# Optimization experiments

Measured on AMD Instinct MI355X. Metric: run time of the kernel, lower is better.

The kernel has to match this reference:

```python
import jax, jax.numpy as jnp
import numpy as np

B, T, I, H, V = 32, 64, 512, 512, 32000


def setup_inputs() -> dict:
    key = jax.random.key(0)
    ks = jax.random.split(key, 8)
    s_in = 1.0 / np.sqrt(H)  # torch LSTMCell/Linear uniform init scale
    return {
        "isequence": jax.random.normal(ks[0], (B, T, I), dtype=jnp.float32),
        "hidden_t": jax.random.normal(ks[1], (B, H), dtype=jnp.float32),
        "W_ih": jax.random.uniform(ks[2], (4 * H, I), jnp.float32, -s_in, s_in),
        "W_hh": jax.random.uniform(ks[3], (4 * H, H), jnp.float32, -s_in, s_in),
        "b_ih": jax.random.uniform(ks[4], (4 * H,), jnp.float32, -s_in, s_in),
        "b_hh": jax.random.uniform(ks[5], (4 * H,), jnp.float32, -s_in, s_in),
        "W_out": jax.random.uniform(ks[6], (V, H), jnp.float32, -s_in, s_in),
        "b_out": jax.random.uniform(ks[7], (V,), jnp.float32, -s_in, s_in),
    }


def reference(isequence, hidden_t, W_ih, W_hh, b_ih, b_hh, W_out, b_out):
    # isequence: [B, T, I] -> time-major [T, B, I] (matches permute(1,0,2))
    xs = jnp.transpose(isequence, (1, 0, 2))
    # Precompute input-to-gate projections for all timesteps: [T, B, 4H]
    x_gates = jnp.einsum("tbi,gi->tbg", xs, W_ih) + b_ih + b_hh
    c0 = jnp.zeros_like(hidden_t)  # init_hidden zeros cell state

    def step(carry, xg):
        h, c = carry
        gates = xg + h @ W_hh.T  # [B, 4H], torch gate order: i, f, g, o
        i_g, f_g, g_g, o_g = jnp.split(gates, 4, axis=-1)
        i_g = jax.nn.sigmoid(i_g)
        f_g = jax.nn.sigmoid(f_g)
        g_g = jnp.tanh(g_g)
        o_g = jax.nn.sigmoid(o_g)
        c_new = f_g * c + i_g * g_g
        h_new = o_g * jnp.tanh(c_new)
        logits = h_new @ W_out.T + b_out  # [B, V]
        return (h_new, c_new), logits

    _, osequence = jax.lax.scan(step, (hidden_t, c0), x_gates)  # [T, B, V]
    return jnp.transpose(osequence, (1, 0, 2))  # [B, T, V]
```

## Files before the change

### kernel.cpp

```cpp
#include <hip/hip_runtime.h>
#include <hip/hip_bf16.h>

typedef unsigned short u16;
typedef unsigned int u32;
typedef __attribute__((ext_vector_type(4))) float f32x4;
typedef __attribute__((ext_vector_type(8))) short short8;
typedef __attribute__((ext_vector_type(4))) unsigned short u16x4;
typedef __attribute__((ext_vector_type(4))) unsigned int u32x4;

#define LSTM_NBLK 16

static __device__ __forceinline__ u16 f2bf(float f) {
  union { float f; unsigned u; } v; v.f = f;
  unsigned r = v.u + 0x7FFFu + ((v.u >> 16) & 1u);
  return (u16)(r >> 16);
}

static __device__ __forceinline__ void gload_lds16(const void* g, void* l) {
  __builtin_amdgcn_global_load_lds(
      (const __attribute__((address_space(1))) unsigned int*)g,
      (__attribute__((address_space(3))) unsigned int*)l, 16, 0, 0);
}

static __device__ __forceinline__ short8 ld_b128_sc(const void* p) {
  short8 r;
  asm volatile("global_load_dwordx4 %0, %1, off sc0 sc1"
               : "=v"(r) : "v"(p) : "memory");
  return r;
}
static __device__ __forceinline__ unsigned ld_u32_sc_wait(const unsigned* p) {
  unsigned r;
  asm volatile("global_load_dword %0, %1, off sc0 sc1\n\ts_waitcnt vmcnt(0)"
               : "=v"(r) : "v"(p) : "memory");
  return r;
}
static __device__ __forceinline__ void st_u32_sc(void* p, unsigned v) {
  asm volatile("global_store_dword %0, %1, off sc0 sc1"
               :: "v"(p), "v"(v) : "memory");
}
static __device__ __forceinline__ void waitcnt0() {
  asm volatile("s_waitcnt vmcnt(0)" ::: "memory");
  __builtin_amdgcn_sched_barrier(0);
}

__global__ void prep_kernel(const float* __restrict__ iseq, const float* __restrict__ h0,
                            const float* __restrict__ wih, const float* __restrict__ whh,
                            const float* __restrict__ wout,
                            u16* __restrict__ wout_bf, u16* __restrict__ wih_bf,
                            u16* __restrict__ whh_bf, u16* __restrict__ ax,
                            u32* __restrict__ h2u, unsigned* __restrict__ flags) {
  const int S0 = 4096000;
  const int S1 = S0 + 262144;
  const int S2 = S1 + 262144;
  const int S3 = S2 + 262144;
  const int S4 = S3 + 8192;
  const int S5 = S4 + 4096;
  int u = blockIdx.x * blockDim.x + threadIdx.x;
  int stride = gridDim.x * blockDim.x;
  for (; u < S5; u += stride) {
    if (u < S0) {
      int e = u * 4; f32x4 v = *(const f32x4*)(wout + e);
      u16x4 o; o[0]=f2bf(v[0]); o[1]=f2bf(v[1]); o[2]=f2bf(v[2]); o[3]=f2bf(v[3]);
      *(u16x4*)(wout_bf + e) = o;
    } else if (u < S1) {
      int e = (u - S0) * 4; f32x4 v = *(const f32x4*)(wih + e);
      u16x4 o; o[0]=f2bf(v[0]); o[1]=f2bf(v[1]); o[2]=f2bf(v[2]); o[3]=f2bf(v[3]);
      *(u16x4*)(wih_bf + e) = o;
    } else if (u < S2) {
      int e = (u - S1) * 4; f32x4 v = *(const f32x4*)(whh + e);
      u16x4 o; o[0]=f2bf(v[0]); o[1]=f2bf(v[1]); o[2]=f2bf(v[2]); o[3]=f2bf(v[3]);
      *(u16x4*)(whh_bf + e) = o;
    } else if (u < S3) {
      int e = (u - S2) * 4; int m = e >> 9; int k = e & 511;
      int b = m & 31; int t = m >> 5;
      f32x4 v = *(const f32x4*)(iseq + ((b * 64 + t) << 9) + k);
      u16x4 o; o[0]=f2bf(v[0]); o[1]=f2bf(v[1]); o[2]=f2bf(v[2]); o[3]=f2bf(v[3]);
      *(u16x4*)(ax + e) = o;
    } else if (u < S4) {
      int v = u - S3;
      int e = v * 2;
      float lo = h0[e], hi = h0[e + 1];
      h2u[v] = (((u32)f2bf(hi)) << 16) | (u32)f2bf(lo);
    } else {
      flags[u - S4] = 0u;
    }
  }
}

__global__ __launch_bounds__(256, 2) void gemm_bt(
    const u16* __restrict__ A, const u16* __restrict__ Bw,
    float* __restrict__ C, const float* __restrict__ bias1,
    const float* __restrict__ bias2, int N, int remap) {
  __shared__ u16 As[2][8192];
  __shared__ u16 Bs[2][8192];
  const int tid = threadIdx.x;
  const int w = tid >> 6, l = tid & 63;
  const int wr = w >> 1, wc = w & 1;
  const int tm = blockIdx.y * 128, tn = blockIdx.x * 128;

  f32x4 acc[4][4];
#pragma unroll
  for (int i = 0; i < 4; ++i)
#pragma unroll
    for (int j = 0; j < 4; ++j) acc[i][j] = (f32x4){0.f, 0.f, 0.f, 0.f};

  auto stage = [&](int buf, int kt) {
#pragma unroll
    for (int i = 0; i < 4; ++i) {
      int r = (w * 4 + i) * 8 + (l >> 3);
      int c16 = (l & 7) ^ (r & 7);
      int rowm = tm + r;
      const u16* srca;
      if (remap) {
        srca = A + ((rowm & 63) + 1) * 16384 + (rowm >> 6) * 512 + kt * 64 + c16 * 8;
      } else {
        srca = A + rowm * 512 + kt * 64 + c16 * 8;
      }
      gload_lds16(srca, &As[buf][(w * 4 + i) * 512]);
      const u16* srcb = Bw + (tn + r) * 512 + kt * 64 + c16 * 8;
      gload_lds16(srcb, &Bs[buf][(w * 4 + i) * 512]);
    }
  };

  stage(0, 0);
  int buf = 0;
  for (int kt = 0; kt < 8; ++kt) {
    __syncthreads();
    if (kt < 7) stage(buf ^ 1, kt + 1);
#pragma unroll
    for (int kk = 0; kk < 2; ++kk) {
      short8 af[4], bfr[4];
#pragma unroll
      for (int mi = 0; mi < 4; ++mi) {
        int row = wr * 64 + mi * 16 + (l & 15);
        int s = (kk * 4 + (l >> 4)) ^ (row & 7);
        af[mi] = *(const short8*)&As[buf][row * 64 + s * 8];
      }
#pragma unroll
      for (int ni = 0; ni < 4; ++ni) {
        int row = wc * 64 + ni * 16 + (l & 15);
        int s = (kk * 4 + (l >> 4)) ^ (row & 7);
        bfr[ni] = *(const short8*)&Bs[buf][row * 64 + s * 8];
      }
#pragma unroll
      for (int mi = 0; mi < 4; ++mi)
#pragma unroll
        for (int ni = 0; ni < 4; ++ni)
          acc[mi][ni] = __builtin_amdgcn_mfma_f32_16x16x32_bf16(
              af[mi], bfr[ni], acc[mi][ni], 0, 0, 0);
    }
    buf ^= 1;
  }

#pragma unroll
  for (int ni = 0; ni < 4; ++ni) {
    int gcol = tn + wc * 64 + ni * 16 + (l & 15);
    float bv = 0.f;
    if (bias1) bv += bias1[gcol];
    if (bias2) bv += bias2[gcol];
#pragma unroll
    for (int mi = 0; mi < 4; ++mi) {
      int grow0 = tm + wr * 64 + mi * 16 + ((l >> 4) << 2);
      f32x4 a = acc[mi][ni];
#pragma unroll
      for (int q = 0; q < 4; ++q) {
        C[(long long)(grow0 + q) * N + gcol] = a[q] + bv;
      }
    }
  }
}

__global__ __launch_bounds__(512, 1) void lstm_persist(
    const u16* __restrict__ whh, const float* __restrict__ xg,
    u16* __restrict__ h2, unsigned* __restrict__ flags) {
  __shared__ u16 hbuf[32 * 512];
  __shared__ u16 hloc[1024];
  const int tid = threadIdx.x;
  const int w = tid >> 6, l = tid & 63;
  const int blk = blockIdx.x;
  const int j0 = (blk * 8 + w) * 4;
  const int c = l & 15;
  const int wrow = (c >> 2) * 512 + j0 + (c & 3);
  const int ko = (l >> 4) * 8;
  u32* h2u = (u32*)h2;

  short8 bfr[16];
  const u16* wp = whh + wrow * 512 + ko;
#pragma unroll
  for (int kt = 0; kt < 16; ++kt) bfr[kt] = *(const short8*)(wp + kt * 32);

  const int rq = (l >> 4) * 4;
  const int jj = l & 3;
  const int b0 = l & 15, b1 = 16 + (l & 15);
  const int s0 = b0 & 7;

  const int cb = tid & 31;
  const int ckg = tid >> 5;
  const int csw = cb & 7;

  const int ob = tid >> 4;
  const int oj = tid & 15;

  float creg[2][4];
#pragma unroll
  for (int mt = 0; mt < 2; ++mt)
#pragma unroll
    for (int q = 0; q < 4; ++q) creg[mt][q] = 0.f;

  float xcur[2][4], xnext[2][4];
#pragma unroll
  for (int mt = 0; mt < 2; ++mt)
#pragma unroll
    for (int q = 0; q < 4; ++q)
      xcur[mt][q] = xg[(mt * 16 + rq + q) * 2048 + wrow];

  for (int it = 0; it < 64; ++it) {
    if (it > 0 && w == 0) {
      const unsigned want = (unsigned)it;
      for (;;) {
        unsigned f = ld_u32_sc_wait(flags + blk * 256 + (l & 15) * 16);
        if (__all((int)(f >= want))) break;
      }
    }
    __syncthreads();

    {
      const u16* src = h2 + it * 16384 + cb * 512 + ckg * 32;
      short8 d0 = ld_b128_sc(src);
      short8 d1 = ld_b128_sc(src + 8);
      short8 d2 = ld_b128_sc(src + 16);
      short8 d3 = ld_b128_sc(src + 24);
      waitcnt0();
      *(short8*)&hbuf[cb * 512 + (((ckg * 4 + 0) ^ csw) * 8)] = d0;
      *(short8*)&hbuf[cb * 512 + (((ckg * 4 + 1) ^ csw) * 8)] = d1;
      *(short8*)&hbuf[cb * 512 + (((ckg * 4 + 2) ^ csw) * 8)] = d2;
      *(short8*)&hbuf[cb * 512 + (((ckg * 4 + 3) ^ csw) * 8)] = d3;
    }
    __syncthreads();

    f32x4 acc0 = (f32x4){0.f, 0.f, 0.f, 0.f};
    f32x4 acc1 = (f32x4){0.f, 0.f, 0.f, 0.f};
#pragma unroll
    for (int kt = 0; kt < 16; ++kt) {
      int x = ((kt * 4 + (l >> 4)) ^ s0) * 8;
      short8 a0 = *(const short8*)&hbuf[b0 * 512 + x];
      short8 a1 = *(const short8*)&hbuf[b1 * 512 + x];
      acc0 = __builtin_amdgcn_mfma_f32_16x16x32_bf16(a0, bfr[kt], acc0, 0, 0, 0);
      acc1 = __builtin_amdgcn_mfma_f32_16x16x32_bf16(a1, bfr[kt], acc1, 0, 0, 0);
    }
    if (it < 63) {
#pragma unroll
      for (int mt = 0; mt < 2; ++mt)
#pragma unroll
        for (int q = 0; q < 4; ++q)
          xnext[mt][q] = xg[((it + 1) * 32 + mt * 16 + rq + q) * 2048 + wrow];
    }

#pragma unroll
    for (int mt = 0; mt < 2; ++mt) {
#pragma unroll
      for (int q = 0; q < 4; ++q) {
        float av = (mt == 0) ? acc0[q] : acc1[q];
        float gp = av + xcur[mt][q];
        int bl = (l & 48) | jj;
        float xi = __shfl(gp, bl);
        float xf = __shfl(gp, bl | 4);
        float xgg = __shfl(gp, bl | 8);
        float xo = __shfl(gp, bl | 12);
        float is = 1.f / (1.f + __expf(-xi));
        float fs = 1.f / (1.f + __expf(-xf));
        float e2 = __expf(2.f * xgg);
        float gt = 1.f - 2.f / (e2 + 1.f);
        float os = 1.f / (1.f + __expf(-xo));
        float cn = fs * creg[mt][q] + is * gt;
        creg[mt][q] = cn;
        float e2c = __expf(2.f * cn);
        float hn = os * (1.f - 2.f / (e2c + 1.f));
        if ((l & 12) == 0) {
          int b = mt * 16 + rq + q;
          hloc[b * 32 + w * 4 + jj] = f2bf(hn);
        }
      }
    }
    __syncthreads();

    {
      u32 v = *(const u32*)&hloc[ob * 32 + oj * 2];
      st_u32_sc(h2u + (it + 1) * 8192 + ob * 256 + blk * 16 + oj, v);
      waitcnt0();
    }
    __syncthreads();

    if (it < 63) {
      if (w == 0 && l < 16)
        st_u32_sc(flags + l * 256 + blk * 16, (unsigned)(it + 1));
#pragma unroll
      for (int mt = 0; mt < 2; ++mt)
#pragma unroll
        for (int q = 0; q < 4; ++q)
          xcur[mt][q] = xnext[mt][q];
    }
  }
}

extern "C" void kernel_launch(void* const* d_in, const int* in_sizes, int n_in,
                              void* d_out, int out_size, void* d_ws, size_t ws_size,
                              hipStream_t stream) {
  (void)in_sizes; (void)n_in; (void)out_size; (void)ws_size;
  const float* iseq = (const float*)d_in[0];
  const float* h0   = (const float*)d_in[1];
  const float* wih  = (const float*)d_in[2];
  const float* whh  = (const float*)d_in[3];
  const float* bih  = (const float*)d_in[4];
  const float* bhh  = (const float*)d_in[5];
  const float* wout = (const float*)d_in[6];
  const float* bout = (const float*)d_in[7];

  char* ws = (char*)d_ws;
  u16* wout_bf = (u16*)(ws + 0);
  u16* wih_bf  = (u16*)(ws + 32768000);
  u16* whh_bf  = (u16*)(ws + 34865152);
  u16* ax      = (u16*)(ws + 36962304);
  u16* h2      = (u16*)(ws + 39059456);
  unsigned* flags = (unsigned*)(ws + 41189376);
  float* xg    = (float*)(ws + 41254912);
  float* out   = (float*)d_out;

  prep_kernel<<<4096, 256, 0, stream>>>(iseq, h0, wih, whh, wout,
                                        wout_bf, wih_bf, whh_bf, ax,
                                        (u32*)h2, flags);
  gemm_bt<<<dim3(16, 16), 256, 0, stream>>>(ax, wih_bf, xg, bih, bhh, 2048, 0);
  lstm_persist<<<LSTM_NBLK, 512, 0, stream>>>(whh_bf, xg, h2, flags);
  gemm_bt<<<dim3(250, 16), 256, 0, stream>>>(h2, wout_bf, out, bout, nullptr, 32000, 1);
}
```

Before: 575.5 us.

## Fuse output projection into persistent LSTM kernel, overlapping it with recurrence

New measurement: 779.0 us. 1.35x slower.

```diff
diff --git a/kernel.cpp b/kernel.cpp
--- a/kernel.cpp
+++ b/kernel.cpp
@@ -9,6 +9,7 @@
 typedef __attribute__((ext_vector_type(4))) unsigned int u32x4;
 
 #define LSTM_NBLK 16
+#define PROJ_NBLK 250
 
 static __device__ __forceinline__ u16 f2bf(float f) {
   union { float f; unsigned u; } v; v.f = f;
@@ -90,7 +91,7 @@
 __global__ __launch_bounds__(256, 2) void gemm_bt(
     const u16* __restrict__ A, const u16* __restrict__ Bw,
     float* __restrict__ C, const float* __restrict__ bias1,
-    const float* __restrict__ bias2, int N, int remap) {
+    const float* __restrict__ bias2, int N) {
   __shared__ u16 As[2][8192];
   __shared__ u16 Bs[2][8192];
   const int tid = threadIdx.x;
@@ -109,13 +110,7 @@
     for (int i = 0; i < 4; ++i) {
       int r = (w * 4 + i) * 8 + (l >> 3);
       int c16 = (l & 7) ^ (r & 7);
-      int rowm = tm + r;
-      const u16* srca;
-      if (remap) {
-        srca = A + ((rowm & 63) + 1) * 16384 + (rowm >> 6) * 512 + kt * 64 + c16 * 8;
-      } else {
-        srca = A + rowm * 512 + kt * 64 + c16 * 8;
-      }
+      const u16* srca = A + (tm + r) * 512 + kt * 64 + c16 * 8;
       gload_lds16(srca, &As[buf][(w * 4 + i) * 512]);
       const u16* srcb = Bw + (tn + r) * 512 + kt * 64 + c16 * 8;
       gload_lds16(srcb, &Bs[buf][(w * 4 + i) * 512]);
@@ -170,62 +165,169 @@
   }
 }
 
-__global__ __launch_bounds__(512, 1) void lstm_persist(
+__global__ __launch_bounds__(512, 1) void fused_persist(
     const u16* __restrict__ whh, const float* __restrict__ xg,
-    u16* __restrict__ h2, unsigned* __restrict__ flags) {
+    u16* __restrict__ h2, unsigned* __restrict__ flags,
+    const u16* __restrict__ woutb, const float* __restrict__ bout,
+    float* __restrict__ out) {
   __shared__ u16 hbuf[32 * 512];
   __shared__ u16 hloc[1024];
   const int tid = threadIdx.x;
   const int w = tid >> 6, l = tid & 63;
-  const int blk = blockIdx.x;
-  const int j0 = (blk * 8 + w) * 4;
-  const int c = l & 15;
-  const int wrow = (c >> 2) * 512 + j0 + (c & 3);
-  const int ko = (l >> 4) * 8;
   u32* h2u = (u32*)h2;
 
-  short8 bfr[16];
-  const u16* wp = whh + wrow * 512 + ko;
-#pragma unroll
-  for (int kt = 0; kt < 16; ++kt) bfr[kt] = *(const short8*)(wp + kt * 32);
-
-  const int rq = (l >> 4) * 4;
-  const int jj = l & 3;
-  const int b0 = l & 15, b1 = 16 + (l & 15);
-  const int s0 = b0 & 7;
+  if (blockIdx.x < LSTM_NBLK) {
+    const int blk = blockIdx.x;
+    const int j0 = (blk * 8 + w) * 4;
+    const int c = l & 15;
+    const int wrow = (c >> 2) * 512 + j0 + (c & 3);
+    const int ko = (l >> 4) * 8;
+
+    short8 bfr[16];
+    const u16* wp = whh + wrow * 512 + ko;
+#pragma unroll
+    for (int kt = 0; kt < 16; ++kt) bfr[kt] = *(const short8*)(wp + kt * 32);
+
+    const int rq = (l >> 4) * 4;
+    const int jj = l & 3;
+    const int b0 = l & 15, b1 = 16 + (l & 15);
+    const int s0 = b0 & 7;
+
+    const int cb = tid & 31;
+    const int ckg = tid >> 5;
+    const int csw = cb & 7;
+    const int ob = tid >> 4;
+    const int oj = tid & 15;
+
+    float creg[2][4];
+#pragma unroll
+    for (int mt = 0; mt < 2; ++mt)
+#pragma unroll
+      for (int q = 0; q < 4; ++q) creg[mt][q] = 0.f;
+
+    float xcur[2][4], xnext[2][4];
+#pragma unroll
+    for (int mt = 0; mt < 2; ++mt)
+#pragma unroll
+      for (int q = 0; q < 4; ++q)
+        xcur[mt][q] = xg[(mt * 16 + rq + q) * 2048 + wrow];
+
+    for (int it = 0; it < 64; ++it) {
+      if (it > 0 && w == 0) {
+        const unsigned want = (unsigned)it;
+        for (;;) {
+          unsigned f = ld_u32_sc_wait(flags + blk * 256 + (l & 15) * 16);
+          if (__all((int)(f >= want))) break;
+        }
+      }
+      __syncthreads();
+
+      {
+        const u16* src = h2 + it * 16384 + cb * 512 + ckg * 32;
+        short8 d0 = ld_b128_sc(src);
+        short8 d1 = ld_b128_sc(src + 8);
+        short8 d2 = ld_b128_sc(src + 16);
+        short8 d3 = ld_b128_sc(src + 24);
+        waitcnt0();
+        *(short8*)&hbuf[cb * 512 + (((ckg * 4 + 0) ^ csw) * 8)] = d0;
+        *(short8*)&hbuf[cb * 512 + (((ckg * 4 + 1) ^ csw) * 8)] = d1;
+        *(short8*)&hbuf[cb * 512 + (((ckg * 4 + 2) ^ csw) * 8)] = d2;
+        *(short8*)&hbuf[cb * 512 + (((ckg * 4 + 3) ^ csw) * 8)] = d3;
+      }
+      __syncthreads();
+
+      f32x4 acc0 = (f32x4){0.f, 0.f, 0.f, 0.f};
+      f32x4 acc1 = (f32x4){0.f, 0.f, 0.f, 0.f};
+#pragma unroll
+      for (int kt = 0; kt < 16; ++kt) {
+        int x = ((kt * 4 + (l >> 4)) ^ s0) * 8;
+        short8 a0 = *(const short8*)&hbuf[b0 * 512 + x];
+        short8 a1 = *(const short8*)&hbuf[b1 * 512 + x];
+        acc0 = __builtin_amdgcn_mfma_f32_16x16x32_bf16(a0, bfr[kt], acc0, 0, 0, 0);
+        acc1 = __builtin_amdgcn_mfma_f32_16x16x32_bf16(a1, bfr[kt], acc1, 0, 0, 0);
+      }
+      if (it < 63) {
+#pragma unroll
+        for (int mt = 0; mt < 2; ++mt)
+#pragma unroll
+          for (int q = 0; q < 4; ++q)
+            xnext[mt][q] = xg[((it + 1) * 32 + mt * 16 + rq + q) * 2048 + wrow];
+      }
+
+#pragma unroll
+      for (int mt = 0; mt < 2; ++mt) {
+#pragma unroll
+        for (int q = 0; q < 4; ++q) {
+          float av = (mt == 0) ? acc0[q] : acc1[q];
+          float gp = av + xcur[mt][q];
+          int bl = (l & 48) | jj;
+          float xi = __shfl(gp, bl);
+          float xf = __shfl(gp, bl | 4);
+          float xgg = __shfl(gp, bl | 8);
+          float xo = __shfl(gp, bl | 12);
+          float is = 1.f / (1.f + __expf(-xi));
+          float fs = 1.f / (1.f + __expf(-xf));
+          float e2 = __expf(2.f * xgg);
+          float gt = 1.f - 2.f / (e2 + 1.f);
+          float os = 1.f / (1.f + __expf(-xo));
+          float cn = fs * creg[mt][q] + is * gt;
+          creg[mt][q] = cn;
+          float e2c = __expf(2.f * cn);
+          float hn = os * (1.f - 2.f / (e2c + 1.f));
+          if ((l & 12) == 0) {
+            int b = mt * 16 + rq + q;
+            hloc[b * 32 + w * 4 + jj] = f2bf(hn);
+          }
+        }
+      }
+      __syncthreads();
+
+      {
+        u32 v = *(const u32*)&hloc[ob * 32 + oj * 2];
+        st_u32_sc(h2u + (it + 1) * 8192 + ob * 256 + blk * 16 + oj, v);
+        waitcnt0();
+      }
+      __syncthreads();
+
+      if (w == 0 && l < 16)
+        st_u32_sc(flags + l * 256 + blk * 16, (unsigned)(it + 1));
+      if (it < 63) {
+#pragma unroll
+        for (int mt = 0; mt < 2; ++mt)
+#pragma unroll
+          for (int q = 0; q < 4; ++q)
+            xcur[mt][q] = xnext[mt][q];
+      }
+    }
+    return;
+  }
+
+  const int pidx = blockIdx.x - LSTM_NBLK;
+  const int c0 = pidx * 128;
+  const int col = c0 + w * 16 + (l & 15);
+  const float bv = bout[col];
+  const u16* bp = woutb + (long long)col * 512 + (l >> 4) * 8;
 
   const int cb = tid & 31;
   const int ckg = tid >> 5;
   const int csw = cb & 7;
-
-  const int ob = tid >> 4;
-  const int oj = tid & 15;
-
-  float creg[2][4];
-#pragma unroll
-  for (int mt = 0; mt < 2; ++mt)
-#pragma unroll
-    for (int q = 0; q < 4; ++q) creg[mt][q] = 0.f;
-
-  float xcur[2][4], xnext[2][4];
-#pragma unroll
-  for (int mt = 0; mt < 2; ++mt)
-#pragma unroll
-    for (int q = 0; q < 4; ++q)
-      xcur[mt][q] = xg[(mt * 16 + rq + q) * 2048 + wrow];
-
-  for (int it = 0; it < 64; ++it) {
-    if (it > 0 && w == 0) {
-      const unsigned want = (unsigned)it;
+  const int b0 = l & 15, b1 = 16 + (l & 15);
+  const int s0 = b0 & 7;
+  const int rq = (l >> 4) * 4;
+  const unsigned* prow = flags + (pidx & 15) * 256;
+
+  for (int t = 0; t < 64; ++t) {
+    if (w == 0) {
+      const unsigned want = (unsigned)(t + 1);
       for (;;) {
-        unsigned f = ld_u32_sc_wait(flags + blk * 256 + (l & 15) * 16);
+        unsigned f = ld_u32_sc_wait(prow + (l & 15) * 16);
         if (__all((int)(f >= want))) break;
       }
     }
     __syncthreads();
 
     {
-      const u16* src = h2 + it * 16384 + cb * 512 + ckg * 32;
+      const u16* src = h2 + (t + 1) * 16384 + cb * 512 + ckg * 32;
       short8 d0 = ld_b128_sc(src);
       short8 d1 = ld_b128_sc(src + 8);
       short8 d2 = ld_b128_sc(src + 16);
@@ -238,67 +340,22 @@
     }
     __syncthreads();
 
-    f32x4 acc0 = (f32x4){0.f, 0.f, 0.f, 0.f};
-    f32x4 acc1 = (f32x4){0.f, 0.f, 0.f, 0.f};
+    f32x4 a0 = (f32x4){0.f, 0.f, 0.f, 0.f};
+    f32x4 a1 = (f32x4){0.f, 0.f, 0.f, 0.f};
 #pragma unroll
     for (int kt = 0; kt < 16; ++kt) {
+      short8 bf = *(const short8*)(bp + kt * 32);
       int x = ((kt * 4 + (l >> 4)) ^ s0) * 8;
-      short8 a0 = *(const short8*)&hbuf[b0 * 512 + x];
-      short8 a1 = *(const short8*)&hbuf[b1 * 512 + x];
-      acc0 = __builtin_amdgcn_mfma_f32_16x16x32_bf16(a0, bfr[kt], acc0, 0, 0, 0);
-      acc1 = __builtin_amdgcn_mfma_f32_16x16x32_bf16(a1, bfr[kt], acc1, 0, 0, 0);
-    }
-    if (it < 63) {
-#pragma unroll
-      for (int mt = 0; mt < 2; ++mt)
-#pragma unroll
-        for (int q = 0; q < 4; ++q)
-          xnext[mt][q] = xg[((it + 1) * 32 + mt * 16 + rq + q) * 2048 + wrow];
-    }
-
-#pragma unroll
-    for (int mt = 0; mt < 2; ++mt) {
-#pragma unroll
-      for (int q = 0; q < 4; ++q) {
-        float av = (mt == 0) ? acc0[q] : acc1[q];
-        float gp = av + xcur[mt][q];
-        int bl = (l & 48) | jj;
-        float xi = __shfl(gp, bl);
-        float xf = __shfl(gp, bl | 4);
-        float xgg = __shfl(gp, bl | 8);
-        float xo = __shfl(gp, bl | 12);
-        float is = 1.f / (1.f + __expf(-xi));
-        float fs = 1.f / (1.f + __expf(-xf));
-        float e2 = __expf(2.f * xgg);
-        float gt = 1.f - 2.f / (e2 + 1.f);
-        float os = 1.f / (1.f + __expf(-xo));
-        float cn = fs * creg[mt][q] + is * gt;
-        creg[mt][q] = cn;
-        float e2c = __expf(2.f * cn);
-        float hn = os * (1.f - 2.f / (e2c + 1.f));
-        if ((l & 12) == 0) {
-          int b = mt * 16 + rq + q;
-          hloc[b * 32 + w * 4 + jj] = f2bf(hn);
-        }
-      }
-    }
-    __syncthreads();
-
-    {
-      u32 v = *(const u32*)&hloc[ob * 32 + oj * 2];
-      st_u32_sc(h2u + (it + 1) * 8192 + ob * 256 + blk * 16 + oj, v);
-      waitcnt0();
-    }
-    __syncthreads();
-
-    if (it < 63) {
-      if (w == 0 && l < 16)
-        st_u32_sc(flags + l * 256 + blk * 16, (unsigned)(it + 1));
-#pragma unroll
-      for (int mt = 0; mt < 2; ++mt)
-#pragma unroll
-        for (int q = 0; q < 4; ++q)
-          xcur[mt][q] = xnext[mt][q];
+      short8 h0f = *(const short8*)&hbuf[b0 * 512 + x];
+      short8 h1f = *(const short8*)&hbuf[b1 * 512 + x];
+      a0 = __builtin_amdgcn_mfma_f32_16x16x32_bf16(h0f, bf, a0, 0, 0, 0);
+      a1 = __builtin_amdgcn_mfma_f32_16x16x32_bf16(h1f, bf, a1, 0, 0, 0);
+    }
+#pragma unroll
+    for (int q = 0; q < 4; ++q) {
+      int br0 = rq + q, br1 = 16 + rq + q;
+      out[(long long)(br0 * 64 + t) * 32000 + col] = a0[q] + bv;
+      out[(long long)(br1 * 64 + t) * 32000 + col] = a1[q] + bv;
     }
   }
 }
@@ -329,7 +386,7 @@
   prep_kernel<<<4096, 256, 0, stream>>>(iseq, h0, wih, whh, wout,
                                         wout_bf, wih_bf, whh_bf, ax,
                                         (u32*)h2, flags);
-  gemm_bt<<<dim3(16, 16), 256, 0, stream>>>(ax, wih_bf, xg, bih, bhh, 2048, 0);
-  lstm_persist<<<LSTM_NBLK, 512, 0, stream>>>(whh_bf, xg, h2, flags);
-  gemm_bt<<<dim3(250, 16), 256, 0, stream>>>(h2, wout_bf, out, bout, nullptr, 32000, 1);
-}
+  gemm_bt<<<dim3(16, 16), 256, 0, stream>>>(ax, wih_bf, xg, bih, bhh, 2048);
+  fused_persist<<<LSTM_NBLK + PROJ_NBLK, 512, 0, stream>>>(
+      whh_bf, xg, h2, flags, wout_bf, bout, out);
+}
```
